# Optimization experiments

Measured on AMD Instinct MI355X. Metric: run time of the kernel, lower is better.

Reference implementation:

```python
import jax, jax.numpy as jnp
import numpy as np

B, S, D_MODEL = 2, 1024, 1024
N_HEADS, D_QK, D_V = 16, 64, 64
MAX_ROPE, MAX_REL = 2048, 128
ATTN_SCALE = 8.0  # sqrt(d_qk)
BASE = 10000.0


def _rope_table():
    # sinusoidal buffer from RoPE.__init__ (pos_type='sinusoidal')
    pos = np.arange(MAX_ROPE).reshape(-1, 1)
    ang = pos / np.power(BASE, np.arange(0, D_QK, 2).reshape(1, -1) / D_QK)
    W = np.zeros((MAX_ROPE, D_QK), dtype=np.float32)
    W[:, 0::2] = np.sin(ang)
    W[:, 1::2] = np.cos(ang)
    return jnp.asarray(W)


def _apply_rope(x, pe):
    # x: [b,n,s,d], pe: [b,s,d]
    cos = jnp.tile(pe[:, :, 1::2], (1, 1, 2))[:, None, :, :]  # [b,1,s,d]
    sin = jnp.tile(pe[:, :, 0::2], (1, 1, 2))[:, None, :, :]
    half = D_QK // 2
    x2 = jnp.concatenate([-x[..., half:], x[..., :half]], axis=-1)
    return x * cos + x2 * sin


def setup_inputs() -> dict:
    key = jax.random.key(0)
    ks = jax.random.split(key, 12)
    w_scale = 1.0 / np.sqrt(D_MODEL)
    inp = {
        'query': jax.random.normal(ks[0], (B, S, D_MODEL), jnp.float32),
        'key': jax.random.normal(ks[1], (B, S, D_MODEL), jnp.float32),
        'value': jax.random.normal(ks[2], (B, S, D_MODEL), jnp.float32),
        'attn_mask': jnp.broadcast_to(jnp.triu(jnp.ones((S, S), bool), 1), (B, S, S)),
        'q_pos_ids': jnp.broadcast_to(jnp.arange(S, dtype=jnp.int32), (B, S)),
        'kv_pos_ids': jnp.broadcast_to(jnp.arange(S, dtype=jnp.int32), (B, S)),
        'W_q': jax.random.normal(ks[3], (N_HEADS * D_QK, D_MODEL), jnp.float32) * w_scale,
        'b_q': jnp.zeros((N_HEADS * D_QK,), jnp.float32),
        'W_k': jax.random.normal(ks[4], (N_HEADS * D_QK, D_MODEL), jnp.float32) * w_scale,
        'b_k': jnp.zeros((N_HEADS * D_QK,), jnp.float32),
        'W_v': jax.random.normal(ks[5], (N_HEADS * D_V, D_MODEL), jnp.float32) * w_scale,
        'b_v': jnp.zeros((N_HEADS * D_V,), jnp.float32),
        'W_o': jax.random.normal(ks[6], (D_MODEL, N_HEADS * D_V), jnp.float32) * w_scale,
        'b_o': jnp.zeros((D_MODEL,), jnp.float32),
        'rel_k_table': jax.random.normal(ks[7], (2 * MAX_REL + 1, D_QK), jnp.float32) * 0.02,
        'rel_v_table': jax.random.normal(ks[8], (2 * MAX_REL + 1, D_V), jnp.float32) * 0.02,
        'w_pre': jax.random.normal(ks[9], (N_HEADS, N_HEADS), jnp.float32) * (1.0 / np.sqrt(N_HEADS)),
        'w_post': jax.random.normal(ks[10], (N_HEADS, N_HEADS), jnp.float32) * (1.0 / np.sqrt(N_HEADS)),
    }
    return inp


def reference(query, key, value, attn_mask, q_pos_ids, kv_pos_ids,
              W_q, b_q, W_k, b_k, W_v, b_v, W_o, b_o,
              rel_k_table, rel_v_table, w_pre, w_post):
    # projections: F.linear(x, W) = x @ W.T, then + bias
    q = (query @ W_q.T + b_q).reshape(B, S, N_HEADS, D_QK).transpose(0, 2, 1, 3)
    k = (key @ W_k.T + b_k).reshape(B, S, N_HEADS, D_QK).transpose(0, 2, 1, 3)
    v = (value @ W_v.T + b_v).reshape(B, S, N_HEADS, D_V).transpose(0, 2, 1, 3)

    # RoPE (sinusoidal buffer, no grad)
    rope_W = _rope_table()
    q = _apply_rope(q, rope_W[q_pos_ids])
    k = _apply_rope(k, rope_W[kv_pos_ids])

    # relative position embeddings (learned tables)
    rel_dis = q_pos_ids[:, :, None] - kv_pos_ids[:, None, :]        # [b,q,k]
    idx = jnp.clip(rel_dis, -MAX_REL, MAX_REL) + MAX_REL
    pos_key = rel_k_table[idx]                                       # [b,q,k,d_qk]
    pos_value = rel_v_table[idx]                                     # [b,q,k,d_v]

    scores = jnp.einsum('bnqd,bnkd->bnqk', q, k)
    scores = scores + jnp.einsum('bnqd,bqkd->bnqk', q, pos_key)
    scores = scores / ATTN_SCALE
    scores = jnp.einsum('bnqk,nm->bmqk', scores, w_pre)              # talking heads pre-softmax
    scores = jnp.where(attn_mask[:, None, :, :], -10000.0, scores)
    attn = jax.nn.softmax(scores, axis=-1)
    attn = jnp.einsum('bmqk,mn->bnqk', attn, w_post)                 # talking heads post-softmax

    out = jnp.einsum('bnqk,bnkd->bnqd', attn, v)
    out = out + jnp.einsum('bnqk,bqkd->bnqd', attn, pos_value)

    out = out.transpose(0, 2, 1, 3).reshape(B, S, N_HEADS * D_V)
    out = out @ W_o.T + b_o
    return out
```

## Files before the change

### kernel.cpp

```cpp
#include <hip/hip_runtime.h>

#define SEQ 1024

typedef short v8s __attribute__((ext_vector_type(8)));
typedef float v4f __attribute__((ext_vector_type(4)));

__device__ __forceinline__ short f2bfs(float f){
  unsigned int u = __float_as_uint(f);
  u += 0x7fffu + ((u >> 16) & 1u);
  return (short)(u >> 16);
}
__device__ __forceinline__ float bfl(short s){
  return __uint_as_float(((unsigned int)(unsigned short)s) << 16);
}

__global__ __launch_bounds__(256) void conv_kernel(
    const float* __restrict__ q, const float* __restrict__ k, const float* __restrict__ v,
    const float* __restrict__ wq, const float* __restrict__ wk2, const float* __restrict__ wv2,
    const float* __restrict__ wo, unsigned short* __restrict__ dst, float* __restrict__ rope)
{
  int bx = blockIdx.x;
  if (bx >= 5120){
    int idx = (bx - 5120) * 256 + threadIdx.x;
    int pos = idx >> 5, i = idx & 31;
    double freq = exp2(-13.287712379549449 * (double)i / 32.0);
    double a = (double)pos * freq;
    rope[pos * 64 + i]      = (float)cos(a);
    rope[pos * 64 + 32 + i] = (float)sin(a);
    return;
  }
  size_t e0 = ((size_t)bx * 256 + threadIdx.x) * 8;
  const float* src; size_t off;
  if      (e0 <  2097152){ src = q;   off = e0; }
  else if (e0 <  4194304){ src = k;   off = e0 - 2097152; }
  else if (e0 <  6291456){ src = v;   off = e0 - 4194304; }
  else if (e0 <  7340032){ src = wq;  off = e0 - 6291456; }
  else if (e0 <  8388608){ src = wk2; off = e0 - 7340032; }
  else if (e0 <  9437184){ src = wv2; off = e0 - 8388608; }
  else                   { src = wo;  off = e0 - 9437184; }
  float4 a = *(const float4*)(src + off);
  float4 b = *(const float4*)(src + off + 4);
  v8s o = { f2bfs(a.x), f2bfs(a.y), f2bfs(a.z), f2bfs(a.w),
            f2bfs(b.x), f2bfs(b.y), f2bfs(b.z), f2bfs(b.w) };
  *(v8s*)(dst + e0) = o;
}

__device__ __forceinline__ void gemm_body(
    const unsigned short* __restrict__ A16,
    const unsigned short* __restrict__ P1, const unsigned short* __restrict__ P2,
    const unsigned short* __restrict__ P3,
    const unsigned short* __restrict__ W16,
    const float* __restrict__ bias, void* __restrict__ outv,
    const float* __restrict__ rope, const int* __restrict__ pos_ids, int mode)
{
  __shared__ short As[2][64][40];
  __shared__ short Ws[2][128][40];

  int t = threadIdx.x;
  int lane = t & 63, wave = t >> 6;
  int l15 = lane & 15, quad = lane >> 4;
  int wm = wave >> 1, wn = wave & 1;
  int row0 = blockIdx.y << 6;
  int col0 = blockIdx.x << 7;

  v4f acc[4];
  #pragma unroll
  for (int j = 0; j < 4; j++) acc[j] = (v4f){0.f, 0.f, 0.f, 0.f};

  int ar = t >> 2, ac = (t & 3) * 8;
  int wr = t >> 2, wc = (t & 3) * 8;
  size_t abase = (size_t)(row0 + ar)*1024 + ac;
  size_t wbase = (size_t)(col0 + wr)*1024 + wc;

  if (t < 256){
    if (P1){
      v8s x0 = *(const v8s*)(A16 + abase);
      v8s x1 = *(const v8s*)(P1 + abase);
      v8s x2 = *(const v8s*)(P2 + abase);
      v8s x3 = *(const v8s*)(P3 + abase);
      v8s o;
      #pragma unroll
      for (int jj = 0; jj < 8; jj++)
        o[jj] = f2bfs(bfl(x0[jj]) + bfl(x1[jj]) + bfl(x2[jj]) + bfl(x3[jj]));
      *(v8s*)&As[0][ar][ac] = o;
    } else {
      *(v8s*)&As[0][ar][ac] = *(const v8s*)(A16 + abase);
    }
  }
  *(v8s*)&Ws[0][wr][wc] = *(const v8s*)(W16 + wbase);
  __syncthreads();

  int cur = 0;
  for (int kt = 0; kt < 1024; kt += 32){
    bool nxt = (kt + 32) < 1024;
    v8s a_st, x1s, x2s, x3s, w_st;
    if (nxt){
      if (t < 256){
        a_st = *(const v8s*)(A16 + abase + kt + 32);
        if (P1){
          x1s = *(const v8s*)(P1 + abase + kt + 32);
          x2s = *(const v8s*)(P2 + abase + kt + 32);
          x3s = *(const v8s*)(P3 + abase + kt + 32);
        }
      }
      w_st = *(const v8s*)(W16 + wbase + kt + 32);
    }

    v8s af = *(v8s*)&As[cur][wm*16 + l15][quad*8];
    v8s bfq[4];
    #pragma unroll
    for (int j = 0; j < 4; j++) bfq[j] = *(v8s*)&Ws[cur][wn*64 + j*16 + l15][quad*8];
    #pragma unroll
    for (int j = 0; j < 4; j++)
      acc[j] = __builtin_amdgcn_mfma_f32_16x16x32_bf16(af, bfq[j], acc[j], 0, 0, 0);

    if (nxt){
      if (t < 256){
        if (P1){
          v8s o;
          #pragma unroll
          for (int jj = 0; jj < 8; jj++)
            o[jj] = f2bfs(bfl(a_st[jj]) + bfl(x1s[jj]) + bfl(x2s[jj]) + bfl(x3s[jj]));
          *(v8s*)&As[cur ^ 1][ar][ac] = o;
        } else {
          *(v8s*)&As[cur ^ 1][ar][ac] = a_st;
        }
      }
      *(v8s*)&Ws[cur ^ 1][wr][wc] = w_st;
      __syncthreads();
      cur ^= 1;
    }
  }

  int rbase = row0 + wm*16 + quad*4;
  if (mode == 1){
    unsigned short* o16 = (unsigned short*)outv;
    int pos[4];
    #pragma unroll
    for (int r = 0; r < 4; r++){
      int p = pos_ids[rbase + r];
      pos[r] = p < 0 ? 0 : (p > 2047 ? 2047 : p);
    }
    #pragma unroll
    for (int j = 0; j < 4; j++){
      int gcol = col0 + wn*64 + j*16 + l15;
      float bs = bias[gcol];
      float bp = bias[gcol ^ 32];
      int idx = (j & 1)*16 + l15;
      #pragma unroll
      for (int r = 0; r < 4; r++){
        float x = acc[j][r] + bs;
        float p = acc[j ^ 2][r] + bp;
        float cs = rope[pos[r]*64 + idx];
        float sn = rope[pos[r]*64 + 32 + idx];
        float o = (j < 2) ? (x*cs - p*sn) : (x*cs + p*sn);
        o16[(size_t)(rbase + r)*1024 + gcol] = (unsigned short)f2bfs(o);
      }
    }
  } else if (mode == 2){
    unsigned short* o16 = (unsigned short*)outv;
    int bb = rbase >> 10, s0 = rbase & 1023;
    #pragma unroll
    for (int j = 0; j < 4; j++){
      int gcol = col0 + wn*64 + j*16 + l15;
      float bs = bias[gcol];
      unsigned int w0 = ((unsigned int)(unsigned short)f2bfs(acc[j][0] + bs)) |
                        (((unsigned int)(unsigned short)f2bfs(acc[j][1] + bs)) << 16);
      unsigned int w1 = ((unsigned int)(unsigned short)f2bfs(acc[j][2] + bs)) |
                        (((unsigned int)(unsigned short)f2bfs(acc[j][3] + bs)) << 16);
      uint2 pk; pk.x = w0; pk.y = w1;
      *(uint2*)&o16[((size_t)(bb*1024 + gcol))*1024 + s0] = pk;
    }
  } else {
    float* o32 = (float*)outv;
    #pragma unroll
    for (int j = 0; j < 4; j++){
      int gcol = col0 + wn*64 + j*16 + l15;
      float bs = bias[gcol];
      #pragma unroll
      for (int r = 0; r < 4; r++)
        o32[(size_t)(rbase + r)*1024 + gcol] = acc[j][r] + bs;
    }
  }
}

__global__ __launch_bounds__(512) void gemm_qkv_kernel(
    const unsigned short* __restrict__ qa, const unsigned short* __restrict__ ka,
    const unsigned short* __restrict__ va,
    const unsigned short* __restrict__ wq, const unsigned short* __restrict__ wk,
    const unsigned short* __restrict__ wv,
    const float* __restrict__ bq, const float* __restrict__ bk, const float* __restrict__ bv,
    unsigned short* __restrict__ oq, unsigned short* __restrict__ ok, unsigned short* __restrict__ ov,
    const float* __restrict__ rope, const int* __restrict__ qpos, const int* __restrict__ kpos)
{
  int z = blockIdx.z;
  const unsigned short* A16 = (z == 0) ? qa : (z == 1) ? ka : va;
  const unsigned short* W16 = (z == 0) ? wq : (z == 1) ? wk : wv;
  const float* bias         = (z == 0) ? bq : (z == 1) ? bk : bv;
  unsigned short* outp      = (z == 0) ? oq : (z == 1) ? ok : ov;
  const int* pos            = (z == 1) ? kpos : qpos;
  int mode                  = (z == 2) ? 2 : 1;
  gemm_body(A16, nullptr, nullptr, nullptr, W16, bias, (void*)outp, rope, pos, mode);
}

__global__ __launch_bounds__(512) void gemm_o_kernel(
    const unsigned short* __restrict__ c0, const unsigned short* __restrict__ c1,
    const unsigned short* __restrict__ c2, const unsigned short* __restrict__ c3,
    const unsigned short* __restrict__ wo, const float* __restrict__ bo,
    float* __restrict__ outp)
{
  gemm_body(c0, c1, c2, c3, wo, bo, (void*)outp, nullptr, nullptr, 0);
}

__global__ __launch_bounds__(1024) void attn_pass1(
    const unsigned short* __restrict__ qw, const unsigned short* __restrict__ kw,
    const float* __restrict__ relk, const float* __restrict__ wpre_g,
    unsigned short* __restrict__ Sp, float* __restrict__ Lp)
{
  __shared__ short U_t[2][512][20];
  __shared__ short W_l[16][16][48];
  __shared__ short relk_s[129][68];

  int t = threadIdx.x;
  int h = t >> 6, lane = t & 63;
  int l15 = lane & 15, quad = lane >> 4;
  int bid = blockIdx.x;
  int quarter = bid & 3;
  int b = (bid >> 2) & 1;
  int qt = 63 - (bid >> 3);
  int q0 = qt << 4;
  int nkt = (qt + 2) >> 1;
  int hq = qt >> 1;
  int offt = hq*(hq+1) + ((qt & 1) ? (hq + 1) : 0);
  unsigned short* Sbase = Sp + ((size_t)(b*1056 + offt)) * 8192;

  for (int e = t; e < 129*64; e += 1024)
    relk_s[e >> 6][e & 63] = f2bfs(relk[(size_t)(128 + (e >> 6))*64 + (e & 63)]);

  v8s awp;
  #pragma unroll
  for (int jj = 0; jj < 8; jj++){
    int n = quad*8 + jj;
    awp[jj] = (n < 16) ? f2bfs(wpre_g[n*16 + l15]) : (short)0;
  }
  v8s aq[2];
  {
    const unsigned short* qb = qw + ((size_t)(b*SEQ + q0 + l15))*1024 + h*64;
    #pragma unroll
    for (int c = 0; c < 2; c++) aq[c] = *(const v8s*)(qb + c*32 + quad*8);
  }
  __syncthreads();

  v4f cinf = (v4f){0.f,0.f,0.f,0.f};
  #pragma unroll
  for (int c = 0; c < 2; c++){
    v8s binf = *(v8s*)&relk_s[128][c*32 + quad*8];
    cinf = __builtin_amdgcn_mfma_f32_16x16x32_bf16(aq[c], binf, cinf, 0, 0, 0);
  }

  float l_part[4] = {0.f, 0.f, 0.f, 0.f};

  v8s kc[2][2];
  if (quarter < nkt){
    int k0 = quarter << 5;
    #pragma unroll
    for (int ct = 0; ct < 2; ct++){
      const unsigned short* kb = kw + ((size_t)(b*SEQ + k0 + ct*16 + l15))*1024 + h*64;
      #pragma unroll
      for (int c = 0; c < 2; c++) kc[ct][c] = *(const v8s*)(kb + c*32 + quad*8);
    }
  }

  int buf = 0;
  for (int ci = quarter; ci < nkt; ci += 4){
    int k0 = ci << 5;
    int r_lo = q0 - k0 - 31;
    bool far = (r_lo >= 128);

    v4f cqk[2];
    #pragma unroll
    for (int ct = 0; ct < 2; ct++){
      v4f acc = (v4f){0.f,0.f,0.f,0.f};
      #pragma unroll
      for (int c = 0; c < 2; c++)
        acc = __builtin_amdgcn_mfma_f32_16x16x32_bf16(aq[c], kc[ct][c], acc, 0, 0, 0);
      cqk[ct] = acc;
    }
    {
      int cin = ci + 4;
      int k0n = ((cin < nkt) ? cin : ci) << 5;
      #pragma unroll
      for (int ct = 0; ct < 2; ct++){
        const unsigned short* kb = kw + ((size_t)(b*SEQ + k0n + ct*16 + l15))*1024 + h*64;
        #pragma unroll
        for (int c = 0; c < 2; c++) kc[ct][c] = *(const v8s*)(kb + c*32 + quad*8);
      }
    }

    if (!far){
      #pragma unroll
      for (int pt = 0; pt < 3; pt++){
        int rr = r_lo + pt*16 + l15; rr = rr < 0 ? 0 : (rr > 128 ? 128 : rr);
        v4f acc = (v4f){0.f,0.f,0.f,0.f};
        #pragma unroll
        for (int c = 0; c < 2; c++){
          v8s rv = *(v8s*)&relk_s[rr][c*32 + quad*8];
          acc = __builtin_amdgcn_mfma_f32_16x16x32_bf16(aq[c], rv, acc, 0, 0, 0);
        }
        #pragma unroll
        for (int reg = 0; reg < 4; reg++)
          W_l[h][quad*4 + reg][pt*16 + l15] = f2bfs(acc[reg]);
      }
    }
    #pragma unroll
    for (int ct = 0; ct < 2; ct++)
      #pragma unroll
      for (int reg = 0; reg < 4; reg++){
        int i = quad*4 + reg, j = ct*16 + l15;
        float wv = far ? cinf[reg] : bfl(W_l[h][i][i - j + 31]);
        U_t[buf][i*32 + j][h] = f2bfs((cqk[ct][reg] + wv) * 0.125f);
      }
    __syncthreads();

    v4f cs[2];
    #pragma unroll
    for (int ct = 0; ct < 2; ct++){
      v8s bu = (v8s){0,0,0,0,0,0,0,0};
      if (quad < 2) bu = *(v8s*)&U_t[buf][h*32 + ct*16 + l15][quad*8];
      cs[ct] = __builtin_amdgcn_mfma_f32_16x16x32_bf16(awp, bu, (v4f){0.f,0.f,0.f,0.f}, 0, 0, 0);
    }
    short sb[2][4];
    unsigned short* stile = Sbase + (size_t)ci * 8192;
    #pragma unroll
    for (int ct = 0; ct < 2; ct++){
      #pragma unroll
      for (int reg = 0; reg < 4; reg++) sb[ct][reg] = f2bfs(cs[ct][reg]);
      uint2 pk;
      pk.x = ((unsigned int)(unsigned short)sb[ct][0]) | (((unsigned int)(unsigned short)sb[ct][1]) << 16);
      pk.y = ((unsigned int)(unsigned short)sb[ct][2]) | (((unsigned int)(unsigned short)sb[ct][3]) << 16);
      *(uint2*)(stile + ((size_t)((h*2 + ct)*64 + quad*16 + l15))*4) = pk;
    }
    bool v0 = (k0 + l15)      <= (q0 + h);
    bool v1 = (k0 + 16 + l15) <= (q0 + h);
    #pragma unroll
    for (int reg = 0; reg < 4; reg++){
      float p0 = v0 ? __expf(bfl(sb[0][reg])) : 0.f;
      float p1 = v1 ? __expf(bfl(sb[1][reg])) : 0.f;
      l_part[reg] += p0 + p1;
    }
    buf ^= 1;
  }

  #pragma unroll
  for (int reg = 0; reg < 4; reg++){
    float sm = l_part[reg];
    sm += __shfl_xor(sm, 1, 64);
    sm += __shfl_xor(sm, 2, 64);
    sm += __shfl_xor(sm, 4, 64);
    sm += __shfl_xor(sm, 8, 64);
    l_part[reg] = sm;
  }
  size_t pb = ((((size_t)b*64 + qt)*4 + quarter)*16 + h)*16;
  if (l15 == 0){
    #pragma unroll
    for (int reg = 0; reg < 4; reg++)
      Lp[pb + quad*4 + reg] = l_part[reg];
  }
}

__global__ __launch_bounds__(1024) void attn_pass2(
    const unsigned short* __restrict__ Sp, const unsigned short* __restrict__ vwT,
    const float* __restrict__ relv, const float* __restrict__ wpost_g,
    const float* __restrict__ Lp,
    unsigned short* __restrict__ c0, unsigned short* __restrict__ c1,
    unsigned short* __restrict__ c2, unsigned short* __restrict__ c3)
{
  __shared__ short U_t[512][20];
  __shared__ short Pp[2][16][16][40];
  __shared__ short relv_s[129][66];
  __shared__ float il_f[16][17], Srow[16][17];

  int t = threadIdx.x;
  int h = t >> 6, lane = t & 63;
  int l15 = lane & 15, quad = lane >> 4;
  int bid = blockIdx.x;
  int quarter = bid & 3;
  int b = (bid >> 2) & 1;
  int qt = 63 - (bid >> 3);
  int q0 = qt << 4;
  int nkt = (qt + 2) >> 1;
  int hq = qt >> 1;
  int offt = hq*(hq+1) + ((qt & 1) ? (hq + 1) : 0);
  const unsigned short* Sbase = Sp + ((size_t)(b*1056 + offt)) * 8192;
  unsigned short* ctx = (quarter == 0) ? c0 : (quarter == 1) ? c1 : (quarter == 2) ? c2 : c3;

  for (int e = t; e < 129*64; e += 1024)
    relv_s[e >> 6][e & 63] = f2bfs(relv[(size_t)(128 + (e >> 6))*64 + (e & 63)]);
  if (t < 256){
    int i = t >> 4, n = t & 15;
    size_t b0 = ((((size_t)b*64 + qt)*4 + 0)*16 + i)*16 + n;
    float l = 0.f;
    #pragma unroll
    for (int qd = 0; qd < 4; qd++) l += Lp[b0 + qd*256];
    il_f[i][n] = 1.f / l;
  }
  v8s awq;
  #pragma unroll
  for (int jj = 0; jj < 8; jj++){
    int n = quad*8 + jj;
    awq[jj] = (n < 16) ? f2bfs(wpost_g[n*16 + l15]) : (short)0;
  }
  __syncthreads();

  v4f o_acc[4];
  #pragma unroll
  for (int dt = 0; dt < 4; dt++) o_acc[dt] = (v4f){0.f,0.f,0.f,0.f};
  float sr_part[4] = {0.f, 0.f, 0.f, 0.f};

  const unsigned short* vtb = vwT + ((size_t)(b*1024 + h*64))*1024;

  uint4 sv;
  if (quarter < nkt) sv = *(const uint4*)(Sbase + (size_t)quarter*8192 + (size_t)t*8);

  int pbuf = 0;
  for (int ci = quarter; ci < nkt; ci += 4){
    int k0 = ci << 5;
    int r_lo = q0 - k0 - 31;
    bool far = (r_lo >= 128);

    #pragma unroll
    for (int g = 0; g < 2; g++){
      unsigned int w0 = (g == 0) ? sv.x : sv.z;
      unsigned int w1 = (g == 0) ? sv.y : sv.w;
      int v = t*2 + g;
      int i = v >> 7, ct = (v >> 6) & 1, quadv = (v >> 4) & 3, lv = v & 15;
      int j = ct*16 + lv;
      bool valid = (k0 + j) <= (q0 + i);
      short at[4];
      unsigned short ss[4] = { (unsigned short)(w0 & 0xffff), (unsigned short)(w0 >> 16),
                               (unsigned short)(w1 & 0xffff), (unsigned short)(w1 >> 16) };
      #pragma unroll
      for (int reg = 0; reg < 4; reg++){
        int n = quadv*4 + reg;
        float a = valid ? __expf(bfl((short)ss[reg])) * il_f[i][n] : 0.f;
        at[reg] = f2bfs(a);
      }
      unsigned int lo = ((unsigned int)(unsigned short)at[0]) | (((unsigned int)(unsigned short)at[1]) << 16);
      unsigned int hi = ((unsigned int)(unsigned short)at[2]) | (((unsigned int)(unsigned short)at[3]) << 16);
      uint2 pk; pk.x = lo; pk.y = hi;
      *(uint2*)&U_t[i*32 + j][quadv*4] = pk;
    }

    v4f cp[2];
    #pragma unroll
    for (int ct = 0; ct < 2; ct++){
      v8s bu = (v8s){0,0,0,0,0,0,0,0};
      if (quad < 2) bu = *(v8s*)&U_t[h*32 + ct*16 + l15][quad*8];
      cp[ct] = __builtin_amdgcn_mfma_f32_16x16x32_bf16(awq, bu, (v4f){0.f,0.f,0.f,0.f}, 0, 0, 0);
    }
    #pragma unroll
    for (int ct = 0; ct < 2; ct++)
      #pragma unroll
      for (int reg = 0; reg < 4; reg++){
        int n = quad*4 + reg, j = ct*16 + l15;
        Pp[pbuf][n][h][j] = f2bfs(cp[ct][reg]);
      }
    if (far){
      #pragma unroll
      for (int reg = 0; reg < 4; reg++)
        sr_part[reg] += cp[0][reg] + cp[1][reg];
    }
    __syncthreads();

    {
      int cin = ci + 4;
      int cld = (cin < nkt) ? cin : ci;
      sv = *(const uint4*)(Sbase + (size_t)cld*8192 + (size_t)t*8);
    }

    v8s ap = *(v8s*)&Pp[pbuf][h][l15][quad*8];
    #pragma unroll
    for (int dt = 0; dt < 4; dt++){
      v8s bv = *(const v8s*)(vtb + (size_t)(dt*16 + l15)*1024 + k0 + quad*8);
      o_acc[dt] = __builtin_amdgcn_mfma_f32_16x16x32_bf16(ap, bv, o_acc[dt], 0, 0, 0);
    }
    if (!far){
      #pragma unroll
      for (int ch = 0; ch < 2; ch++){
        v8s at2;
        #pragma unroll
        for (int jj = 0; jj < 8; jj++){
          int jx = l15 + 31 - (ch*32 + quad*8 + jj);
          at2[jj] = ((unsigned)jx < 32u) ? Pp[pbuf][h][l15][jx] : (short)0;
        }
        #pragma unroll
        for (int dt = 0; dt < 4; dt++){
          v8s br;
          #pragma unroll
          for (int jj = 0; jj < 8; jj++){
            int rr = r_lo + ch*32 + quad*8 + jj;
            rr = rr < 0 ? 0 : (rr > 128 ? 128 : rr);
            br[jj] = relv_s[rr][dt*16 + l15];
          }
          o_acc[dt] = __builtin_amdgcn_mfma_f32_16x16x32_bf16(at2, br, o_acc[dt], 0, 0, 0);
        }
      }
    }
    pbuf ^= 1;
  }

  #pragma unroll
  for (int reg = 0; reg < 4; reg++){
    float s = sr_part[reg];
    s += __shfl_xor(s, 1, 64);
    s += __shfl_xor(s, 2, 64);
    s += __shfl_xor(s, 4, 64);
    s += __shfl_xor(s, 8, 64);
    if (l15 == 0) Srow[quad*4 + reg][h] = s;
  }
  __syncthreads();

  #pragma unroll
  for (int dt = 0; dt < 4; dt++)
    #pragma unroll
    for (int reg = 0; reg < 4; reg++){
      float o = o_acc[dt][reg] + Srow[h][quad*4 + reg] * bfl(relv_s[128][dt*16 + l15]);
      ctx[((size_t)(b*SEQ + q0 + quad*4 + reg))*1024 + h*64 + dt*16 + l15] = (unsigned short)f2bfs(o);
    }
}

extern "C" void kernel_launch(void* const* d_in, const int* in_sizes, int n_in,
                              void* d_out, int out_size, void* d_ws, size_t ws_size,
                              hipStream_t stream)
{
  int ip = -1;
  for (int i = 0; i < n_in; i++){
    if (in_sizes[i] == 2048){ ip = i; break; }
  }
  if (ip < 0) ip = 4;

  const float* query = (const float*)d_in[0];
  const float* key   = (const float*)d_in[1];
  const float* value = (const float*)d_in[2];
  const int* qpos = (const int*)d_in[ip];
  const int* kpos = (const int*)d_in[ip + 1];
  const float* Wq    = (const float*)d_in[ip + 2];
  const float* bq    = (const float*)d_in[ip + 3];
  const float* Wk    = (const float*)d_in[ip + 4];
  const float* bk    = (const float*)d_in[ip + 5];
  const float* Wv    = (const float*)d_in[ip + 6];
  const float* b_v   = (const float*)d_in[ip + 7];
  const float* Wo    = (const float*)d_in[ip + 8];
  const float* bo    = (const float*)d_in[ip + 9];
  const float* relk  = (const float*)d_in[ip + 10];
  const float* relv  = (const float*)d_in[ip + 11];
  const float* wpre  = (const float*)d_in[ip + 12];
  const float* wpost = (const float*)d_in[ip + 13];

  char* ws = (char*)d_ws;
  float* rope           = (float*)ws;
  unsigned short* conv  = (unsigned short*)(ws + 524288);
  unsigned short* qbf   = conv;
  unsigned short* kbf   = conv + 2097152;
  unsigned short* vbf   = conv + 4194304;
  unsigned short* wqbf  = conv + 6291456;
  unsigned short* wkbf  = conv + 7340032;
  unsigned short* wvbf  = conv + 8388608;
  unsigned short* wobf  = conv + 9437184;
  unsigned short* q_ws  = (unsigned short*)(ws + 21495808);
  unsigned short* k_ws  = (unsigned short*)(ws + 25690112);
  unsigned short* v_ws  = (unsigned short*)(ws + 29884416);
  unsigned short* ctx0  = (unsigned short*)(ws + 34078720);
  unsigned short* ctx1  = (unsigned short*)(ws + 38273024);
  unsigned short* ctx2  = (unsigned short*)(ws + 42467328);
  unsigned short* ctx3  = (unsigned short*)(ws + 46661632);
  unsigned short* Sp    = (unsigned short*)(ws + 50855936);
  float* Lp             = (float*)(ws + 85983232);

  hipLaunchKernelGGL(conv_kernel, dim3(5376), dim3(256), 0, stream,
                     query, key, value, Wq, Wk, Wv, Wo, conv, rope);
  hipLaunchKernelGGL(gemm_qkv_kernel, dim3(8, 32, 3), dim3(512), 0, stream,
                     qbf, kbf, vbf, wqbf, wkbf, wvbf, bq, bk, b_v,
                     q_ws, k_ws, v_ws, rope, qpos, kpos);
  hipLaunchKernelGGL(attn_pass1, dim3(512), dim3(1024), 0, stream,
                     q_ws, k_ws, relk, wpre, Sp, Lp);
  hipLaunchKernelGGL(attn_pass2, dim3(512), dim3(1024), 0, stream,
                     Sp, v_ws, relv, wpost, Lp, ctx0, ctx1, ctx2, ctx3);
  hipLaunchKernelGGL(gemm_o_kernel, dim3(8, 32), dim3(512), 0, stream,
                     ctx0, ctx1, ctx2, ctx3, wobf, bo, (float*)d_out);
}
```

Measured before the change: 257.7 us.

## Fuse fp32-to-bf16 conversion into GEMMs, compute RoPE inline, store exp probabilities

Drops the separate conversion/rope kernel. The QKV and output GEMMs now load fp32 activations and weights directly and convert them to bf16 while staging into shared memory. RoPE cos/sin values are computed in registers with fast intrinsics instead of read from a precomputed table, which may cost some accuracy. Pass1 now stores exp'd, masked probabilities so pass2 skips the exp and mask, and pass2 prefetches the V fragments one iteration ahead. Together these cut a launch and a full read/write of the converted buffers, at the price of more fp32 global traffic inside the GEMMs.

```diff
diff --git a/kernel.cpp b/kernel.cpp
--- a/kernel.cpp
+++ b/kernel.cpp
@@ -13,45 +13,19 @@
 __device__ __forceinline__ float bfl(short s){
   return __uint_as_float(((unsigned int)(unsigned short)s) << 16);
 }
-
-__global__ __launch_bounds__(256) void conv_kernel(
-    const float* __restrict__ q, const float* __restrict__ k, const float* __restrict__ v,
-    const float* __restrict__ wq, const float* __restrict__ wk2, const float* __restrict__ wv2,
-    const float* __restrict__ wo, unsigned short* __restrict__ dst, float* __restrict__ rope)
-{
-  int bx = blockIdx.x;
-  if (bx >= 5120){
-    int idx = (bx - 5120) * 256 + threadIdx.x;
-    int pos = idx >> 5, i = idx & 31;
-    double freq = exp2(-13.287712379549449 * (double)i / 32.0);
-    double a = (double)pos * freq;
-    rope[pos * 64 + i]      = (float)cos(a);
-    rope[pos * 64 + 32 + i] = (float)sin(a);
-    return;
-  }
-  size_t e0 = ((size_t)bx * 256 + threadIdx.x) * 8;
-  const float* src; size_t off;
-  if      (e0 <  2097152){ src = q;   off = e0; }
-  else if (e0 <  4194304){ src = k;   off = e0 - 2097152; }
-  else if (e0 <  6291456){ src = v;   off = e0 - 4194304; }
-  else if (e0 <  7340032){ src = wq;  off = e0 - 6291456; }
-  else if (e0 <  8388608){ src = wk2; off = e0 - 7340032; }
-  else if (e0 <  9437184){ src = wv2; off = e0 - 8388608; }
-  else                   { src = wo;  off = e0 - 9437184; }
-  float4 a = *(const float4*)(src + off);
-  float4 b = *(const float4*)(src + off + 4);
+__device__ __forceinline__ v8s cvt8(float4 a, float4 b){
   v8s o = { f2bfs(a.x), f2bfs(a.y), f2bfs(a.z), f2bfs(a.w),
             f2bfs(b.x), f2bfs(b.y), f2bfs(b.z), f2bfs(b.w) };
-  *(v8s*)(dst + e0) = o;
+  return o;
 }
 
 __device__ __forceinline__ void gemm_body(
-    const unsigned short* __restrict__ A16,
-    const unsigned short* __restrict__ P1, const unsigned short* __restrict__ P2,
-    const unsigned short* __restrict__ P3,
-    const unsigned short* __restrict__ W16,
+    const float* __restrict__ A32,
+    const unsigned short* __restrict__ P0, const unsigned short* __restrict__ P1,
+    const unsigned short* __restrict__ P2, const unsigned short* __restrict__ P3,
+    const float* __restrict__ W32,
     const float* __restrict__ bias, void* __restrict__ outv,
-    const float* __restrict__ rope, const int* __restrict__ pos_ids, int mode)
+    const int* __restrict__ pos_ids, int mode)
 {
   __shared__ short As[2][64][40];
   __shared__ short Ws[2][128][40];
@@ -73,8 +47,12 @@
   size_t wbase = (size_t)(col0 + wr)*1024 + wc;
 
   if (t < 256){
-    if (P1){
-      v8s x0 = *(const v8s*)(A16 + abase);
+    if (A32){
+      float4 a0 = *(const float4*)(A32 + abase);
+      float4 a1 = *(const float4*)(A32 + abase + 4);
+      *(v8s*)&As[0][ar][ac] = cvt8(a0, a1);
+    } else {
+      v8s x0 = *(const v8s*)(P0 + abase);
       v8s x1 = *(const v8s*)(P1 + abase);
       v8s x2 = *(const v8s*)(P2 + abase);
       v8s x3 = *(const v8s*)(P3 + abase);
@@ -83,27 +61,34 @@
       for (int jj = 0; jj < 8; jj++)
         o[jj] = f2bfs(bfl(x0[jj]) + bfl(x1[jj]) + bfl(x2[jj]) + bfl(x3[jj]));
       *(v8s*)&As[0][ar][ac] = o;
-    } else {
-      *(v8s*)&As[0][ar][ac] = *(const v8s*)(A16 + abase);
-    }
-  }
-  *(v8s*)&Ws[0][wr][wc] = *(const v8s*)(W16 + wbase);
+    }
+  }
+  {
+    float4 w0 = *(const float4*)(W32 + wbase);
+    float4 w1 = *(const float4*)(W32 + wbase + 4);
+    *(v8s*)&Ws[0][wr][wc] = cvt8(w0, w1);
+  }
   __syncthreads();
 
   int cur = 0;
   for (int kt = 0; kt < 1024; kt += 32){
     bool nxt = (kt + 32) < 1024;
-    v8s a_st, x1s, x2s, x3s, w_st;
+    float4 a0s, a1s, w0s, w1s;
+    v8s x0s, x1s, x2s, x3s;
     if (nxt){
       if (t < 256){
-        a_st = *(const v8s*)(A16 + abase + kt + 32);
-        if (P1){
+        if (A32){
+          a0s = *(const float4*)(A32 + abase + kt + 32);
+          a1s = *(const float4*)(A32 + abase + kt + 36);
+        } else {
+          x0s = *(const v8s*)(P0 + abase + kt + 32);
           x1s = *(const v8s*)(P1 + abase + kt + 32);
           x2s = *(const v8s*)(P2 + abase + kt + 32);
           x3s = *(const v8s*)(P3 + abase + kt + 32);
         }
       }
-      w_st = *(const v8s*)(W16 + wbase + kt + 32);
+      w0s = *(const float4*)(W32 + wbase + kt + 32);
+      w1s = *(const float4*)(W32 + wbase + kt + 36);
     }
 
     v8s af = *(v8s*)&As[cur][wm*16 + l15][quad*8];
@@ -116,17 +101,17 @@
 
     if (nxt){
       if (t < 256){
-        if (P1){
+        if (A32){
+          *(v8s*)&As[cur ^ 1][ar][ac] = cvt8(a0s, a1s);
+        } else {
           v8s o;
           #pragma unroll
           for (int jj = 0; jj < 8; jj++)
-            o[jj] = f2bfs(bfl(a_st[jj]) + bfl(x1s[jj]) + bfl(x2s[jj]) + bfl(x3s[jj]));
+            o[jj] = f2bfs(bfl(x0s[jj]) + bfl(x1s[jj]) + bfl(x2s[jj]) + bfl(x3s[jj]));
           *(v8s*)&As[cur ^ 1][ar][ac] = o;
-        } else {
-          *(v8s*)&As[cur ^ 1][ar][ac] = a_st;
         }
       }
-      *(v8s*)&Ws[cur ^ 1][wr][wc] = w_st;
+      *(v8s*)&Ws[cur ^ 1][wr][wc] = cvt8(w0s, w1s);
       __syncthreads();
       cur ^= 1;
     }
@@ -141,18 +126,27 @@
       int p = pos_ids[rbase + r];
       pos[r] = p < 0 ? 0 : (p > 2047 ? 2047 : p);
     }
+    float fr0 = exp2f(-0.4152410118609203f * (float)l15);
+    float fr1 = exp2f(-0.4152410118609203f * (float)(16 + l15));
+    float csv[2][4], snv[2][4];
+    #pragma unroll
+    for (int r = 0; r < 4; r++){
+      float a0 = (float)pos[r] * fr0;
+      float a1 = (float)pos[r] * fr1;
+      csv[0][r] = __cosf(a0); snv[0][r] = __sinf(a0);
+      csv[1][r] = __cosf(a1); snv[1][r] = __sinf(a1);
+    }
     #pragma unroll
     for (int j = 0; j < 4; j++){
       int gcol = col0 + wn*64 + j*16 + l15;
       float bs = bias[gcol];
       float bp = bias[gcol ^ 32];
-      int idx = (j & 1)*16 + l15;
       #pragma unroll
       for (int r = 0; r < 4; r++){
         float x = acc[j][r] + bs;
         float p = acc[j ^ 2][r] + bp;
-        float cs = rope[pos[r]*64 + idx];
-        float sn = rope[pos[r]*64 + 32 + idx];
+        float cs = csv[j & 1][r];
+        float sn = snv[j & 1][r];
         float o = (j < 2) ? (x*cs - p*sn) : (x*cs + p*sn);
         o16[(size_t)(rbase + r)*1024 + gcol] = (unsigned short)f2bfs(o);
       }
@@ -185,31 +179,29 @@
 }
 
 __global__ __launch_bounds__(512) void gemm_qkv_kernel(
-    const unsigned short* __restrict__ qa, const unsigned short* __restrict__ ka,
-    const unsigned short* __restrict__ va,
-    const unsigned short* __restrict__ wq, const unsigned short* __restrict__ wk,
-    const unsigned short* __restrict__ wv,
+    const float* __restrict__ qa, const float* __restrict__ ka, const float* __restrict__ va,
+    const float* __restrict__ wq, const float* __restrict__ wk, const float* __restrict__ wv,
     const float* __restrict__ bq, const float* __restrict__ bk, const float* __restrict__ bv,
     unsigned short* __restrict__ oq, unsigned short* __restrict__ ok, unsigned short* __restrict__ ov,
-    const float* __restrict__ rope, const int* __restrict__ qpos, const int* __restrict__ kpos)
+    const int* __restrict__ qpos, const int* __restrict__ kpos)
 {
   int z = blockIdx.z;
-  const unsigned short* A16 = (z == 0) ? qa : (z == 1) ? ka : va;
-  const unsigned short* W16 = (z == 0) ? wq : (z == 1) ? wk : wv;
-  const float* bias         = (z == 0) ? bq : (z == 1) ? bk : bv;
-  unsigned short* outp      = (z == 0) ? oq : (z == 1) ? ok : ov;
-  const int* pos            = (z == 1) ? kpos : qpos;
-  int mode                  = (z == 2) ? 2 : 1;
-  gemm_body(A16, nullptr, nullptr, nullptr, W16, bias, (void*)outp, rope, pos, mode);
+  const float* A32 = (z == 0) ? qa : (z == 1) ? ka : va;
+  const float* W32 = (z == 0) ? wq : (z == 1) ? wk : wv;
+  const float* bias = (z == 0) ? bq : (z == 1) ? bk : bv;
+  unsigned short* outp = (z == 0) ? oq : (z == 1) ? ok : ov;
+  const int* pos = (z == 1) ? kpos : qpos;
+  int mode = (z == 2) ? 2 : 1;
+  gemm_body(A32, nullptr, nullptr, nullptr, nullptr, W32, bias, (void*)outp, pos, mode);
 }
 
 __global__ __launch_bounds__(512) void gemm_o_kernel(
     const unsigned short* __restrict__ c0, const unsigned short* __restrict__ c1,
     const unsigned short* __restrict__ c2, const unsigned short* __restrict__ c3,
-    const unsigned short* __restrict__ wo, const float* __restrict__ bo,
+    const float* __restrict__ wo, const float* __restrict__ bo,
     float* __restrict__ outp)
 {
-  gemm_body(c0, c1, c2, c3, wo, bo, (void*)outp, nullptr, nullptr, 0);
+  gemm_body(nullptr, c0, c1, c2, c3, wo, bo, (void*)outp, nullptr, 0);
 }
 
 __global__ __launch_bounds__(1024) void attn_pass1(
@@ -329,24 +321,21 @@
       if (quad < 2) bu = *(v8s*)&U_t[buf][h*32 + ct*16 + l15][quad*8];
       cs[ct] = __builtin_amdgcn_mfma_f32_16x16x32_bf16(awp, bu, (v4f){0.f,0.f,0.f,0.f}, 0, 0, 0);
     }
-    short sb[2][4];
     unsigned short* stile = Sbase + (size_t)ci * 8192;
     #pragma unroll
     for (int ct = 0; ct < 2; ct++){
-      #pragma unroll
-      for (int reg = 0; reg < 4; reg++) sb[ct][reg] = f2bfs(cs[ct][reg]);
+      bool vv = (k0 + ct*16 + l15) <= (q0 + h);
+      short pb16[4];
+      #pragma unroll
+      for (int reg = 0; reg < 4; reg++){
+        float p = vv ? __expf(cs[ct][reg]) : 0.f;
+        l_part[reg] += p;
+        pb16[reg] = f2bfs(p);
+      }
       uint2 pk;
-      pk.x = ((unsigned int)(unsigned short)sb[ct][0]) | (((unsigned int)(unsigned short)sb[ct][1]) << 16);
-      pk.y = ((unsigned int)(unsigned short)sb[ct][2]) | (((unsigned int)(unsigned short)sb[ct][3]) << 16);
+      pk.x = ((unsigned int)(unsigned short)pb16[0]) | (((unsigned int)(unsigned short)pb16[1]) << 16);
+      pk.y = ((unsigned int)(unsigned short)pb16[2]) | (((unsigned int)(unsigned short)pb16[3]) << 16);
       *(uint2*)(stile + ((size_t)((h*2 + ct)*64 + quad*16 + l15))*4) = pk;
-    }
-    bool v0 = (k0 + l15)      <= (q0 + h);
-    bool v1 = (k0 + 16 + l15) <= (q0 + h);
-    #pragma unroll
-    for (int reg = 0; reg < 4; reg++){
-      float p0 = v0 ? __expf(bfl(sb[0][reg])) : 0.f;
-      float p1 = v1 ? __expf(bfl(sb[1][reg])) : 0.f;
-      l_part[reg] += p0 + p1;
     }
     buf ^= 1;
   }
@@ -420,7 +409,14 @@
   const unsigned short* vtb = vwT + ((size_t)(b*1024 + h*64))*1024;
 
   uint4 sv;
-  if (quarter < nkt) sv = *(const uint4*)(Sbase + (size_t)quarter*8192 + (size_t)t*8);
+  v8s bvc[4];
+  if (quarter < nkt){
+    sv = *(const uint4*)(Sbase + (size_t)quarter*8192 + (size_t)t*8);
+    int k0 = quarter << 5;
+    #pragma unroll
+    for (int dt = 0; dt < 4; dt++)
+      bvc[dt] = *(const v8s*)(vtb + (size_t)(dt*16 + l15)*1024 + k0 + quad*8);
+  }
 
   int pbuf = 0;
   for (int ci = quarter; ci < nkt; ci += 4){
@@ -435,15 +431,13 @@
       int v = t*2 + g;
       int i = v >> 7, ct = (v >> 6) & 1, quadv = (v >> 4) & 3, lv = v & 15;
       int j = ct*16 + lv;
-      bool valid = (k0 + j) <= (q0 + i);
       short at[4];
       unsigned short ss[4] = { (unsigned short)(w0 & 0xffff), (unsigned short)(w0 >> 16),
                                (unsigned short)(w1 & 0xffff), (unsigned short)(w1 >> 16) };
       #pragma unroll
       for (int reg = 0; reg < 4; reg++){
         int n = quadv*4 + reg;
-        float a = valid ? __expf(bfl((short)ss[reg])) * il_f[i][n] : 0.f;
-        at[reg] = f2bfs(a);
+        at[reg] = f2bfs(bfl((short)ss[reg]) * il_f[i][n]);
       }
       unsigned int lo = ((unsigned int)(unsigned short)at[0]) | (((unsigned int)(unsigned short)at[1]) << 16);
       unsigned int hi = ((unsigned int)(unsigned short)at[2]) | (((unsigned int)(unsigned short)at[3]) << 16);
@@ -480,9 +474,14 @@
 
     v8s ap = *(v8s*)&Pp[pbuf][h][l15][quad*8];
     #pragma unroll
-    for (int dt = 0; dt < 4; dt++){
-      v8s bv = *(const v8s*)(vtb + (size_t)(dt*16 + l15)*1024 + k0 + quad*8);
-      o_acc[dt] = __builtin_amdgcn_mfma_f32_16x16x32_bf16(ap, bv, o_acc[dt], 0, 0, 0);
+    for (int dt = 0; dt < 4; dt++)
+      o_acc[dt] = __builtin_amdgcn_mfma_f32_16x16x32_bf16(ap, bvc[dt], o_acc[dt], 0, 0, 0);
+    {
+      int cin = ci + 4;
+      int k0n = ((cin < nkt) ? cin : ci) << 5;
+      #pragma unroll
+      for (int dt = 0; dt < 4; dt++)
+        bvc[dt] = *(const v8s*)(vtb + (size_t)(dt*16 + l15)*1024 + k0n + quad*8);
     }
     if (!far){
       #pragma unroll
@@ -558,15 +557,6 @@
   const float* wpost = (const float*)d_in[ip + 13];
 
   char* ws = (char*)d_ws;
-  float* rope           = (float*)ws;
-  unsigned short* conv  = (unsigned short*)(ws + 524288);
-  unsigned short* qbf   = conv;
-  unsigned short* kbf   = conv + 2097152;
-  unsigned short* vbf   = conv + 4194304;
-  unsigned short* wqbf  = conv + 6291456;
-  unsigned short* wkbf  = conv + 7340032;
-  unsigned short* wvbf  = conv + 8388608;
-  unsigned short* wobf  = conv + 9437184;
   unsigned short* q_ws  = (unsigned short*)(ws + 21495808);
   unsigned short* k_ws  = (unsigned short*)(ws + 25690112);
   unsigned short* v_ws  = (unsigned short*)(ws + 29884416);
@@ -577,15 +567,13 @@
   unsigned short* Sp    = (unsigned short*)(ws + 50855936);
   float* Lp             = (float*)(ws + 85983232);
 
-  hipLaunchKernelGGL(conv_kernel, dim3(5376), dim3(256), 0, stream,
-                     query, key, value, Wq, Wk, Wv, Wo, conv, rope);
   hipLaunchKernelGGL(gemm_qkv_kernel, dim3(8, 32, 3), dim3(512), 0, stream,
-                     qbf, kbf, vbf, wqbf, wkbf, wvbf, bq, bk, b_v,
-                     q_ws, k_ws, v_ws, rope, qpos, kpos);
+                     query, key, value, Wq, Wk, Wv, bq, bk, b_v,
+                     q_ws, k_ws, v_ws, qpos, kpos);
   hipLaunchKernelGGL(attn_pass1, dim3(512), dim3(1024), 0, stream,
                      q_ws, k_ws, relk, wpre, Sp, Lp);
   hipLaunchKernelGGL(attn_pass2, dim3(512), dim3(1024), 0, stream,
                      Sp, v_ws, relv, wpost, Lp, ctx0, ctx1, ctx2, ctx3);
   hipLaunchKernelGGL(gemm_o_kernel, dim3(8, 32), dim3(512), 0, stream,
-                     ctx0, ctx1, ctx2, ctx3, wobf, bo, (float*)d_out);
-}
+                     ctx0, ctx1, ctx2, ctx3, Wo, bo, (float*)d_out);
+}
```

After: 263.6 us. 2.3% more time.

## Compute RoPE inline, store exp scores in pass1, prefetch V fragments in pass2

Applied to the files above, without the earlier changes.

Three changes. The RoPE table is no longer precomputed in double precision inside the conversion kernel; each QK GEMM epilogue now computes cos and sin on the fly with fast float intrinsics. Attention pass1 now writes exp(score), masked, as bf16 instead of the raw score, so pass2 no longer needs exp or the causal mask when rebuilding probabilities. Pass2 also prefetches the V MFMA operands for the next chunk into registers. The fast __sinf/__cosf on arguments up to about 1023 and storing probabilities rather than scores in bf16 may change numerical accuracy.

```diff
diff --git a/kernel.cpp b/kernel.cpp
--- a/kernel.cpp
+++ b/kernel.cpp
@@ -17,19 +17,9 @@
 __global__ __launch_bounds__(256) void conv_kernel(
     const float* __restrict__ q, const float* __restrict__ k, const float* __restrict__ v,
     const float* __restrict__ wq, const float* __restrict__ wk2, const float* __restrict__ wv2,
-    const float* __restrict__ wo, unsigned short* __restrict__ dst, float* __restrict__ rope)
-{
-  int bx = blockIdx.x;
-  if (bx >= 5120){
-    int idx = (bx - 5120) * 256 + threadIdx.x;
-    int pos = idx >> 5, i = idx & 31;
-    double freq = exp2(-13.287712379549449 * (double)i / 32.0);
-    double a = (double)pos * freq;
-    rope[pos * 64 + i]      = (float)cos(a);
-    rope[pos * 64 + 32 + i] = (float)sin(a);
-    return;
-  }
-  size_t e0 = ((size_t)bx * 256 + threadIdx.x) * 8;
+    const float* __restrict__ wo, unsigned short* __restrict__ dst)
+{
+  size_t e0 = ((size_t)blockIdx.x * 256 + threadIdx.x) * 8;
   const float* src; size_t off;
   if      (e0 <  2097152){ src = q;   off = e0; }
   else if (e0 <  4194304){ src = k;   off = e0 - 2097152; }
@@ -51,7 +41,7 @@
     const unsigned short* __restrict__ P3,
     const unsigned short* __restrict__ W16,
     const float* __restrict__ bias, void* __restrict__ outv,
-    const float* __restrict__ rope, const int* __restrict__ pos_ids, int mode)
+    const int* __restrict__ pos_ids, int mode)
 {
   __shared__ short As[2][64][40];
   __shared__ short Ws[2][128][40];
@@ -141,18 +131,27 @@
       int p = pos_ids[rbase + r];
       pos[r] = p < 0 ? 0 : (p > 2047 ? 2047 : p);
     }
+    float fr0 = exp2f(-0.4152410118609203f * (float)l15);
+    float fr1 = exp2f(-0.4152410118609203f * (float)(16 + l15));
+    float csv[2][4], snv[2][4];
+    #pragma unroll
+    for (int r = 0; r < 4; r++){
+      float a0 = (float)pos[r] * fr0;
+      float a1 = (float)pos[r] * fr1;
+      csv[0][r] = __cosf(a0); snv[0][r] = __sinf(a0);
+      csv[1][r] = __cosf(a1); snv[1][r] = __sinf(a1);
+    }
     #pragma unroll
     for (int j = 0; j < 4; j++){
       int gcol = col0 + wn*64 + j*16 + l15;
       float bs = bias[gcol];
       float bp = bias[gcol ^ 32];
-      int idx = (j & 1)*16 + l15;
       #pragma unroll
       for (int r = 0; r < 4; r++){
         float x = acc[j][r] + bs;
         float p = acc[j ^ 2][r] + bp;
-        float cs = rope[pos[r]*64 + idx];
-        float sn = rope[pos[r]*64 + 32 + idx];
+        float cs = csv[j & 1][r];
+        float sn = snv[j & 1][r];
         float o = (j < 2) ? (x*cs - p*sn) : (x*cs + p*sn);
         o16[(size_t)(rbase + r)*1024 + gcol] = (unsigned short)f2bfs(o);
       }
@@ -191,7 +190,7 @@
     const unsigned short* __restrict__ wv,
     const float* __restrict__ bq, const float* __restrict__ bk, const float* __restrict__ bv,
     unsigned short* __restrict__ oq, unsigned short* __restrict__ ok, unsigned short* __restrict__ ov,
-    const float* __restrict__ rope, const int* __restrict__ qpos, const int* __restrict__ kpos)
+    const int* __restrict__ qpos, const int* __restrict__ kpos)
 {
   int z = blockIdx.z;
   const unsigned short* A16 = (z == 0) ? qa : (z == 1) ? ka : va;
@@ -200,7 +199,7 @@
   unsigned short* outp      = (z == 0) ? oq : (z == 1) ? ok : ov;
   const int* pos            = (z == 1) ? kpos : qpos;
   int mode                  = (z == 2) ? 2 : 1;
-  gemm_body(A16, nullptr, nullptr, nullptr, W16, bias, (void*)outp, rope, pos, mode);
+  gemm_body(A16, nullptr, nullptr, nullptr, W16, bias, (void*)outp, pos, mode);
 }
 
 __global__ __launch_bounds__(512) void gemm_o_kernel(
@@ -209,7 +208,7 @@
     const unsigned short* __restrict__ wo, const float* __restrict__ bo,
     float* __restrict__ outp)
 {
-  gemm_body(c0, c1, c2, c3, wo, bo, (void*)outp, nullptr, nullptr, 0);
+  gemm_body(c0, c1, c2, c3, wo, bo, (void*)outp, nullptr, 0);
 }
 
 __global__ __launch_bounds__(1024) void attn_pass1(
@@ -329,24 +328,21 @@
       if (quad < 2) bu = *(v8s*)&U_t[buf][h*32 + ct*16 + l15][quad*8];
       cs[ct] = __builtin_amdgcn_mfma_f32_16x16x32_bf16(awp, bu, (v4f){0.f,0.f,0.f,0.f}, 0, 0, 0);
     }
-    short sb[2][4];
     unsigned short* stile = Sbase + (size_t)ci * 8192;
     #pragma unroll
     for (int ct = 0; ct < 2; ct++){
-      #pragma unroll
-      for (int reg = 0; reg < 4; reg++) sb[ct][reg] = f2bfs(cs[ct][reg]);
+      bool vv = (k0 + ct*16 + l15) <= (q0 + h);
+      short pb16[4];
+      #pragma unroll
+      for (int reg = 0; reg < 4; reg++){
+        float p = vv ? __expf(cs[ct][reg]) : 0.f;
+        l_part[reg] += p;
+        pb16[reg] = f2bfs(p);
+      }
       uint2 pk;
-      pk.x = ((unsigned int)(unsigned short)sb[ct][0]) | (((unsigned int)(unsigned short)sb[ct][1]) << 16);
-      pk.y = ((unsigned int)(unsigned short)sb[ct][2]) | (((unsigned int)(unsigned short)sb[ct][3]) << 16);
+      pk.x = ((unsigned int)(unsigned short)pb16[0]) | (((unsigned int)(unsigned short)pb16[1]) << 16);
+      pk.y = ((unsigned int)(unsigned short)pb16[2]) | (((unsigned int)(unsigned short)pb16[3]) << 16);
       *(uint2*)(stile + ((size_t)((h*2 + ct)*64 + quad*16 + l15))*4) = pk;
-    }
-    bool v0 = (k0 + l15)      <= (q0 + h);
-    bool v1 = (k0 + 16 + l15) <= (q0 + h);
-    #pragma unroll
-    for (int reg = 0; reg < 4; reg++){
-      float p0 = v0 ? __expf(bfl(sb[0][reg])) : 0.f;
-      float p1 = v1 ? __expf(bfl(sb[1][reg])) : 0.f;
-      l_part[reg] += p0 + p1;
     }
     buf ^= 1;
   }
@@ -420,7 +416,14 @@
   const unsigned short* vtb = vwT + ((size_t)(b*1024 + h*64))*1024;
 
   uint4 sv;
-  if (quarter < nkt) sv = *(const uint4*)(Sbase + (size_t)quarter*8192 + (size_t)t*8);
+  v8s bvc[4];
+  if (quarter < nkt){
+    sv = *(const uint4*)(Sbase + (size_t)quarter*8192 + (size_t)t*8);
+    int k0 = quarter << 5;
+    #pragma unroll
+    for (int dt = 0; dt < 4; dt++)
+      bvc[dt] = *(const v8s*)(vtb + (size_t)(dt*16 + l15)*1024 + k0 + quad*8);
+  }
 
   int pbuf = 0;
   for (int ci = quarter; ci < nkt; ci += 4){
@@ -435,15 +438,13 @@
       int v = t*2 + g;
       int i = v >> 7, ct = (v >> 6) & 1, quadv = (v >> 4) & 3, lv = v & 15;
       int j = ct*16 + lv;
-      bool valid = (k0 + j) <= (q0 + i);
       short at[4];
       unsigned short ss[4] = { (unsigned short)(w0 & 0xffff), (unsigned short)(w0 >> 16),
                                (unsigned short)(w1 & 0xffff), (unsigned short)(w1 >> 16) };
       #pragma unroll
       for (int reg = 0; reg < 4; reg++){
         int n = quadv*4 + reg;
-        float a = valid ? __expf(bfl((short)ss[reg])) * il_f[i][n] : 0.f;
-        at[reg] = f2bfs(a);
+        at[reg] = f2bfs(bfl((short)ss[reg]) * il_f[i][n]);
       }
       unsigned int lo = ((unsigned int)(unsigned short)at[0]) | (((unsigned int)(unsigned short)at[1]) << 16);
       unsigned int hi = ((unsigned int)(unsigned short)at[2]) | (((unsigned int)(unsigned short)at[3]) << 16);
@@ -480,9 +481,14 @@
 
     v8s ap = *(v8s*)&Pp[pbuf][h][l15][quad*8];
     #pragma unroll
-    for (int dt = 0; dt < 4; dt++){
-      v8s bv = *(const v8s*)(vtb + (size_t)(dt*16 + l15)*1024 + k0 + quad*8);
-      o_acc[dt] = __builtin_amdgcn_mfma_f32_16x16x32_bf16(ap, bv, o_acc[dt], 0, 0, 0);
+    for (int dt = 0; dt < 4; dt++)
+      o_acc[dt] = __builtin_amdgcn_mfma_f32_16x16x32_bf16(ap, bvc[dt], o_acc[dt], 0, 0, 0);
+    {
+      int cin = ci + 4;
+      int k0n = ((cin < nkt) ? cin : ci) << 5;
+      #pragma unroll
+      for (int dt = 0; dt < 4; dt++)
+        bvc[dt] = *(const v8s*)(vtb + (size_t)(dt*16 + l15)*1024 + k0n + quad*8);
     }
     if (!far){
       #pragma unroll
@@ -558,7 +564,6 @@
   const float* wpost = (const float*)d_in[ip + 13];
 
   char* ws = (char*)d_ws;
-  float* rope           = (float*)ws;
   unsigned short* conv  = (unsigned short*)(ws + 524288);
   unsigned short* qbf   = conv;
   unsigned short* kbf   = conv + 2097152;
@@ -577,11 +582,11 @@
   unsigned short* Sp    = (unsigned short*)(ws + 50855936);
   float* Lp             = (float*)(ws + 85983232);
 
-  hipLaunchKernelGGL(conv_kernel, dim3(5376), dim3(256), 0, stream,
-                     query, key, value, Wq, Wk, Wv, Wo, conv, rope);
+  hipLaunchKernelGGL(conv_kernel, dim3(5120), dim3(256), 0, stream,
+                     query, key, value, Wq, Wk, Wv, Wo, conv);
   hipLaunchKernelGGL(gemm_qkv_kernel, dim3(8, 32, 3), dim3(512), 0, stream,
                      qbf, kbf, vbf, wqbf, wkbf, wvbf, bq, bk, b_v,
-                     q_ws, k_ws, v_ws, rope, qpos, kpos);
+                     q_ws, k_ws, v_ws, qpos, kpos);
   hipLaunchKernelGGL(attn_pass1, dim3(512), dim3(1024), 0, stream,
                      q_ws, k_ws, relk, wpre, Sp, Lp);
   hipLaunchKernelGGL(attn_pass2, dim3(512), dim3(1024), 0, stream,
```

New measurement: 248.9 us. 1.04x faster.
